# Kernel tuning notes

Hardware: AMD Instinct MI355X
Metric: run time of the kernel (lower is better)

Reference implementation:

```python
import jax, jax.numpy as jnp
import numpy as np

D_MODEL = 1024
NUM_HEADS = 16


def setup_inputs() -> dict:
    key = jax.random.key(0)
    k_x, k_q, k_k, k_v, k_o = jax.random.split(key, 5)
    std = np.sqrt(2.0 / (D_MODEL + D_MODEL))
    x = jax.random.normal(k_x, (2, 2048, D_MODEL), dtype=jnp.float32)
    # LinearLayer stores weight as (out_features, in_features); forward does x @ W.T
    w_q = std * jax.random.truncated_normal(k_q, -2.0, 2.0, (D_MODEL, D_MODEL), dtype=jnp.float32)
    w_k = std * jax.random.truncated_normal(k_k, -2.0, 2.0, (D_MODEL, D_MODEL), dtype=jnp.float32)
    w_v = std * jax.random.truncated_normal(k_v, -2.0, 2.0, (D_MODEL, D_MODEL), dtype=jnp.float32)
    w_o = std * jax.random.truncated_normal(k_o, -2.0, 2.0, (D_MODEL, D_MODEL), dtype=jnp.float32)
    return {"x": x, "w_q": w_q, "w_k": w_k, "w_v": w_v, "w_o": w_o}


def reference(x, w_q, w_k, w_v, w_o):
    B, S, D = x.shape
    H = NUM_HEADS
    dk = D // H
    # projections: x @ W.T
    def split_heads(t):
        return t.reshape(B, S, H, dk).transpose(0, 2, 1, 3)  # (B,H,S,dk)
    q = split_heads(x @ w_q.T)
    k = split_heads(x @ w_k.T)
    v = split_heads(x @ w_v.T)
    scale = 1.0 / np.sqrt(dk).astype(np.float32)
    score = jnp.einsum('bhqd,bhkd->bhqk', q, k) * scale  # (B,H,S,S)
    causal = jnp.tril(jnp.ones((S, S), dtype=bool))
    score = jnp.where(causal[None, None], score, jnp.float32(-jnp.inf))
    attn = jax.nn.softmax(score, axis=-1)
    out = jnp.einsum('bhqk,bhkd->bhqd', attn, v)  # (B,H,S,dk)
    out = out.transpose(0, 2, 1, 3).reshape(B, S, D)
    return out @ w_o.T
```

## Files before the change

### kernel.cpp

```cpp
#include <hip/hip_runtime.h>
#include <hip/hip_bf16.h>
#include <math.h>

typedef float f32x4 __attribute__((ext_vector_type(4)));
typedef short bf16x8_t __attribute__((ext_vector_type(8)));
typedef unsigned short u16;
typedef unsigned int u32;

#define SEQ     2048
#define DMODEL  1024
#define HEADS   16
#define DK      64

__device__ __forceinline__ u16 f2bf(float f) {
    union { float f; unsigned int u; } x; x.f = f;
    unsigned int r = x.u + 0x7fffu + ((x.u >> 16) & 1u);
    return (u16)(r >> 16);
}

__device__ __forceinline__ float bf2f(u16 v) {
    union { u32 u; float f; } x; x.u = ((u32)v) << 16; return x.f;
}

__device__ __forceinline__ int swz(int row) { return ((row ^ (row >> 3)) & 7) << 4; }

__device__ __forceinline__ void gload_lds16(const u16* g, u16* l) {
    __builtin_amdgcn_global_load_lds((const __attribute__((address_space(1))) void*)g,
                                     (__attribute__((address_space(3))) void*)l,
                                     16, 0, 0);
}

__global__ void cvt5(const float* __restrict__ s0, const float* __restrict__ s1,
                     const float* __restrict__ s2, const float* __restrict__ s3,
                     const float* __restrict__ s4,
                     u16* __restrict__ d0, u16* __restrict__ d1, u16* __restrict__ d2,
                     u16* __restrict__ d3, u16* __restrict__ d4,
                     int n0, int n1, int n2, int n3, int n4)
{
    const float* s; u16* d; int n;
    switch (blockIdx.y) {
        case 0: s = s0; d = d0; n = n0; break;
        case 1: s = s1; d = d1; n = n1; break;
        case 2: s = s2; d = d2; n = n2; break;
        case 3: s = s3; d = d3; n = n3; break;
        default: s = s4; d = d4; n = n4; break;
    }
    int i = (blockIdx.x * 256 + threadIdx.x) * 4;
    if (i >= n) return;
    float4 v = *(const float4*)(s + i);
    ushort4 o;
    o.x = f2bf(v.x); o.y = f2bf(v.y); o.z = f2bf(v.z); o.w = f2bf(v.w);
    *(ushort4*)(d + i) = o;
}

template<int OUTBF16, int BN>
__launch_bounds__(256, 2)
__global__ void gemm_bt(const u16* __restrict__ A,
                        const u16* __restrict__ B0, const u16* __restrict__ B1,
                        const u16* __restrict__ B2,
                        void* C0v, void* C1v, void* C2v,
                        int M, int N, int K)
{
    const u16* B = (blockIdx.z == 0) ? B0 : (blockIdx.z == 1 ? B1 : B2);
    void* Cv     = (blockIdx.z == 0) ? C0v : (blockIdx.z == 1 ? C1v : C2v);

    __shared__ u16 Als[128 * 64];
    __shared__ u16 Bls[BN * 64];

    const int tid = threadIdx.x;
    const int w = tid >> 6, l = tid & 63;
    const int rl = l & 15, rh = l >> 4;
    const int row0 = blockIdx.x * 128, col0 = blockIdx.y * BN;
    constexpr int MI = (BN == 128) ? 4 : 2;
    const int wr = (BN == 128) ? (w >> 1) * 64 : w * 32;
    const int wc = (BN == 128) ? (w & 1) * 64 : 0;

    f32x4 acc[MI][4];
    #pragma unroll
    for (int i = 0; i < MI; i++)
        #pragma unroll
        for (int j = 0; j < 4; j++)
            acc[i][j] = (f32x4){0.f, 0.f, 0.f, 0.f};

    for (int kt = 0; kt < K; kt += 64) {
        #pragma unroll
        for (int i = 0; i < 4; i++) {
            int c = i * 256 + tid;
            int r = c >> 3, s = c & 7;
            gload_lds16(A + (size_t)(row0 + r) * K + kt + s * 8, &Als[(i * 256 + w * 64) * 8]);
        }
        #pragma unroll
        for (int i = 0; i < BN / 32; i++) {
            int c = i * 256 + tid;
            int r = c >> 3, s = c & 7;
            gload_lds16(B + (size_t)(col0 + r) * K + kt + s * 8, &Bls[(i * 256 + w * 64) * 8]);
        }
        __syncthreads();

        bf16x8_t af[MI][2], bfr[4][2];
        #pragma unroll
        for (int mi = 0; mi < MI; mi++)
            #pragma unroll
            for (int k0 = 0; k0 < 2; k0++)
                af[mi][k0] = *(const bf16x8_t*)&Als[(wr + mi * 16 + rl) * 64 + k0 * 32 + rh * 8];
        #pragma unroll
        for (int ni = 0; ni < 4; ni++)
            #pragma unroll
            for (int k0 = 0; k0 < 2; k0++)
                bfr[ni][k0] = *(const bf16x8_t*)&Bls[(wc + ni * 16 + rl) * 64 + k0 * 32 + rh * 8];

        #pragma unroll
        for (int mi = 0; mi < MI; mi++)
            #pragma unroll
            for (int ni = 0; ni < 4; ni++)
                #pragma unroll
                for (int k0 = 0; k0 < 2; k0++)
                    acc[mi][ni] = __builtin_amdgcn_mfma_f32_16x16x32_bf16(
                        af[mi][k0], bfr[ni][k0], acc[mi][ni], 0, 0, 0);
        __syncthreads();
    }

    #pragma unroll
    for (int mi = 0; mi < MI; mi++)
        #pragma unroll
        for (int ni = 0; ni < 4; ni++) {
            int r = row0 + wr + mi * 16 + rh * 4;
            int c = col0 + wc + ni * 16 + rl;
            #pragma unroll
            for (int j = 0; j < 4; j++) {
                if (OUTBF16) ((u16*)Cv)[(size_t)(r + j) * N + c] = f2bf(acc[mi][ni][j]);
                else         ((float*)Cv)[(size_t)(r + j) * N + c] = acc[mi][ni][j];
            }
        }
}

__launch_bounds__(256, 4)
__global__ void attn_fwd(const u16* __restrict__ Q, const u16* __restrict__ Kp,
                         const u16* __restrict__ Vp, u16* __restrict__ O)
{
    const int pi = blockIdx.x;
    const int bh = blockIdx.y;
    const int b = bh >> 4, h = bh & 15;
    const int tid = threadIdx.x, w = tid >> 6, l = tid & 63;
    const int rl = l & 15, rh = l >> 4;

    __shared__ u16 Kls[2][64 * 64];
    __shared__ u16 Vt[2][64 * 64];
    __shared__ u16 Pls[4][16 * 64];

    const size_t base = (size_t)b * SEQ * DMODEL + h * DK;
    const float SC = 0.125f * 1.44269504f;
    const int krl8 = l >> 3, ks = l & 7;
    const int rpair = tid >> 3, dseg = tid & 7;

    for (int half = 0; half < 2; half++) {
        const int qti = half ? (31 - pi) : pi;
        const int nt = qti + 1;
        const int qt0 = qti * 64;

        bf16x8_t qf[2];
        #pragma unroll
        for (int k0 = 0; k0 < 2; k0++) {
            int row = qt0 + w * 16 + rl;
            bf16x8_t qr = *(const bf16x8_t*)(Q + base + (size_t)row * DMODEL + k0 * 32 + rh * 8);
            #pragma unroll
            for (int j = 0; j < 8; j++)
                qf[k0][j] = (short)f2bf(bf2f((u16)qr[j]) * SC);
        }

        f32x4 oacc[4];
        float mrun[4], lrun[4];
        #pragma unroll
        for (int nd = 0; nd < 4; nd++) oacc[nd] = (f32x4){0.f, 0.f, 0.f, 0.f};
        #pragma unroll
        for (int j = 0; j < 4; j++) { mrun[j] = -INFINITY; lrun[j] = 0.f; }

        #pragma unroll
        for (int c = 0; c < 2; c++) {
            int kr = w * 16 + c * 8 + krl8;
            int sseg = ks ^ ((kr ^ (kr >> 3)) & 7);
            gload_lds16(Kp + base + (size_t)kr * DMODEL + sseg * 8,
                        &Kls[0][(w * 16 + c * 8) * 64]);
        }
        {
            const u16* vg = Vp + base + (size_t)(2 * rpair) * DMODEL + dseg * 8;
            bf16x8_t v0 = *(const bf16x8_t*)vg;
            bf16x8_t v1 = *(const bf16x8_t*)(vg + DMODEL);
            #pragma unroll
            for (int j = 0; j < 8; j++) {
                int d = dseg * 8 + j;
                u32 pk = (u32)(u16)v0[j] | ((u32)(u16)v1[j] << 16);
                *(u32*)((char*)&Vt[0][0] + ((d * 128 + rpair * 4) ^ swz(d))) = pk;
            }
        }
        __syncthreads();

        for (int t = 0; t < nt; t++) {
            const int cur = t & 1;
            const bool more = (t + 1 < nt);
            bf16x8_t vv0, vv1;

            if (more) {
                #pragma unroll
                for (int c = 0; c < 2; c++) {
                    int kr = w * 16 + c * 8 + krl8;
                    int sseg = ks ^ ((kr ^ (kr >> 3)) & 7);
                    gload_lds16(Kp + base + (size_t)((t + 1) * 64 + kr) * DMODEL + sseg * 8,
                                &Kls[cur ^ 1][(w * 16 + c * 8) * 64]);
                }
                const u16* vg = Vp + base + (size_t)((t + 1) * 64 + 2 * rpair) * DMODEL + dseg * 8;
                vv0 = *(const bf16x8_t*)vg;
                vv1 = *(const bf16x8_t*)(vg + DMODEL);
            }

            f32x4 sa[4];
            #pragma unroll
            for (int ni = 0; ni < 4; ni++) sa[ni] = (f32x4){0.f, 0.f, 0.f, 0.f};
            #pragma unroll
            for (int k0 = 0; k0 < 2; k0++) {
                bf16x8_t kf[4];
                #pragma unroll
                for (int ni = 0; ni < 4; ni++) {
                    int row = ni * 16 + rl;
                    kf[ni] = *(const bf16x8_t*)((const char*)&Kls[cur][0] +
                              (((row * 64 + k0 * 32 + rh * 8) * 2) ^ swz(row)));
                }
                #pragma unroll
                for (int ni = 0; ni < 4; ni++)
                    sa[ni] = __builtin_amdgcn_mfma_f32_16x16x32_bf16(
                        qf[k0], kf[ni], sa[ni], 0, 0, 0);
            }

            const bool diag = (t + 1 == nt);
            float rmax[4], rsum[4];
            #pragma unroll
            for (int j = 0; j < 4; j++) {
                float mx = -INFINITY;
                #pragma unroll
                for (int ni = 0; ni < 4; ni++) {
                    float s = sa[ni][j];
                    if (diag) {
                        s = ((ni * 16 + rl) > (w * 16 + rh * 4 + j)) ? -INFINITY : s;
                        sa[ni][j] = s;
                    }
                    mx = fmaxf(mx, s);
                }
                rmax[j] = mx;
            }
            #pragma unroll
            for (int msk = 1; msk < 16; msk <<= 1)
                #pragma unroll
                for (int j = 0; j < 4; j++)
                    rmax[j] = fmaxf(rmax[j], __shfl_xor(rmax[j], msk, 64));
            #pragma unroll
            for (int j = 0; j < 4; j++) {
                const float mn = fmaxf(mrun[j], rmax[j]);
                const float alpha = exp2f(mrun[j] - mn);
                mrun[j] = mn;
                float rs = 0.f;
                #pragma unroll
                for (int ni = 0; ni < 4; ni++) {
                    float p = exp2f(sa[ni][j] - mn);
                    sa[ni][j] = p;
                    rs += p;
                }
                rsum[j] = rs;
                lrun[j] *= alpha;
                #pragma unroll
                for (int nd = 0; nd < 4; nd++) oacc[nd][j] *= alpha;
            }
            #pragma unroll
            for (int msk = 1; msk < 16; msk <<= 1)
                #pragma unroll
                for (int j = 0; j < 4; j++)
                    rsum[j] += __shfl_xor(rsum[j], msk, 64);
            #pragma unroll
            for (int j = 0; j < 4; j++) lrun[j] += rsum[j];

            #pragma unroll
            for (int ni = 0; ni < 4; ni++)
                #pragma unroll
                for (int j = 0; j < 4; j++) {
                    int row = rh * 4 + j;
                    *(u16*)((char*)&Pls[w][0] +
                            (((row * 64 + ni * 16 + rl) * 2) ^ swz(row))) = f2bf(sa[ni][j]);
                }

            #pragma unroll
            for (int k0 = 0; k0 < 2; k0++) {
                bf16x8_t pf = *(const bf16x8_t*)((const char*)&Pls[w][0] +
                               (((rl * 64 + k0 * 32 + rh * 8) * 2) ^ swz(rl)));
                bf16x8_t vf[4];
                #pragma unroll
                for (int nd = 0; nd < 4; nd++) {
                    int row = nd * 16 + rl;
                    vf[nd] = *(const bf16x8_t*)((const char*)&Vt[cur][0] +
                              (((row * 64 + k0 * 32 + rh * 8) * 2) ^ swz(row)));
                }
                #pragma unroll
                for (int nd = 0; nd < 4; nd++)
                    oacc[nd] = __builtin_amdgcn_mfma_f32_16x16x32_bf16(
                        pf, vf[nd], oacc[nd], 0, 0, 0);
            }

            if (more) {
                #pragma unroll
                for (int j = 0; j < 8; j++) {
                    int d = dseg * 8 + j;
                    u32 pk = (u32)(u16)vv0[j] | ((u32)(u16)vv1[j] << 16);
                    *(u32*)((char*)&Vt[cur ^ 1][0] + ((d * 128 + rpair * 4) ^ swz(d))) = pk;
                }
            }
            __syncthreads();
        }

        #pragma unroll
        for (int nd = 0; nd < 4; nd++)
            #pragma unroll
            for (int j = 0; j < 4; j++) {
                int row = qt0 + w * 16 + rh * 4 + j;
                O[base + (size_t)row * DMODEL + nd * 16 + rl] =
                    f2bf(oacc[nd][j] / lrun[j]);
            }
    }
}

extern "C" void kernel_launch(void* const* d_in, const int* in_sizes, int n_in,
                              void* d_out, int out_size, void* d_ws, size_t ws_size,
                              hipStream_t stream)
{
    const float* x  = (const float*)d_in[0];
    const float* wq = (const float*)d_in[1];
    const float* wk = (const float*)d_in[2];
    const float* wv = (const float*)d_in[3];
    const float* wo = (const float*)d_in[4];
    float* out = (float*)d_out;

    const size_t NX = (size_t)4096 * 1024;
    const size_t NW = (size_t)1024 * 1024;

    u16* xb  = (u16*)d_ws;
    u16* wqb = xb  + NX;
    u16* wkb = wqb + NW;
    u16* wvb = wkb + NW;
    u16* wob = wvb + NW;
    u16* q   = wob + NW;
    u16* k   = q   + NX;
    u16* v   = k   + NX;
    u16* at  = v   + NX;

    cvt5<<<dim3(4096, 5), 256, 0, stream>>>(x, wq, wk, wv, wo,
                                            xb, wqb, wkb, wvb, wob,
                                            (int)NX, (int)NW, (int)NW, (int)NW, (int)NW);

    gemm_bt<1, 128><<<dim3(32, 8, 3), 256, 0, stream>>>(xb, wqb, wkb, wvb,
                                                        q, k, v, 4096, 1024, 1024);

    attn_fwd<<<dim3(16, 32), 256, 0, stream>>>(q, k, v, at);

    gemm_bt<0, 64><<<dim3(32, 16, 1), 256, 0, stream>>>(at, wob, wob, wob,
                                                        out, out, out, 4096, 1024, 1024);
}
```

Before: 230.5 us.

## Transpose QK^T MFMA, lazy softmax rescaling, and remap block indices

The QK^T MFMA now computes S^T by swapping its operands, so each lane holds one query row. Row max and sum then need only two cross-lane shuffles instead of four per value, and P is written to LDS as packed 32-bit pairs. The running max is rescaled only when some row's max grows by more than 8 (log2 domain), which skips most exp and multiply rescales but lets exponents grow up to 2^8 before correction. Block indices are also remapped so that groups of concurrently scheduled blocks share batch-head K/V data.

```diff
diff --git a/kernel.cpp b/kernel.cpp
--- a/kernel.cpp
+++ b/kernel.cpp
@@ -138,8 +138,9 @@
 __global__ void attn_fwd(const u16* __restrict__ Q, const u16* __restrict__ Kp,
                          const u16* __restrict__ Vp, u16* __restrict__ O)
 {
-    const int pi = blockIdx.x;
-    const int bh = blockIdx.y;
+    const int L  = blockIdx.x + (blockIdx.y << 4);
+    const int pi = L >> 5;
+    const int bh = (((L >> 3) & 3) << 3) | (L & 7);
     const int b = bh >> 4, h = bh & 15;
     const int tid = threadIdx.x, w = tid >> 6, l = tid & 63;
     const int rl = l & 15, rh = l >> 4;
@@ -169,11 +170,9 @@
         }
 
         f32x4 oacc[4];
-        float mrun[4], lrun[4];
+        float mrun = -INFINITY, lrun = 0.f;
         #pragma unroll
         for (int nd = 0; nd < 4; nd++) oacc[nd] = (f32x4){0.f, 0.f, 0.f, 0.f};
-        #pragma unroll
-        for (int j = 0; j < 4; j++) { mrun[j] = -INFINITY; lrun[j] = 0.f; }
 
         #pragma unroll
         for (int c = 0; c < 2; c++) {
@@ -228,63 +227,63 @@
                 #pragma unroll
                 for (int ni = 0; ni < 4; ni++)
                     sa[ni] = __builtin_amdgcn_mfma_f32_16x16x32_bf16(
-                        qf[k0], kf[ni], sa[ni], 0, 0, 0);
-            }
-
-            const bool diag = (t + 1 == nt);
-            float rmax[4], rsum[4];
-            #pragma unroll
-            for (int j = 0; j < 4; j++) {
-                float mx = -INFINITY;
-                #pragma unroll
-                for (int ni = 0; ni < 4; ni++) {
-                    float s = sa[ni][j];
-                    if (diag) {
-                        s = ((ni * 16 + rl) > (w * 16 + rh * 4 + j)) ? -INFINITY : s;
-                        sa[ni][j] = s;
-                    }
-                    mx = fmaxf(mx, s);
-                }
-                rmax[j] = mx;
-            }
-            #pragma unroll
-            for (int msk = 1; msk < 16; msk <<= 1)
-                #pragma unroll
-                for (int j = 0; j < 4; j++)
-                    rmax[j] = fmaxf(rmax[j], __shfl_xor(rmax[j], msk, 64));
-            #pragma unroll
-            for (int j = 0; j < 4; j++) {
-                const float mn = fmaxf(mrun[j], rmax[j]);
-                const float alpha = exp2f(mrun[j] - mn);
-                mrun[j] = mn;
-                float rs = 0.f;
-                #pragma unroll
-                for (int ni = 0; ni < 4; ni++) {
-                    float p = exp2f(sa[ni][j] - mn);
+                        kf[ni], qf[k0], sa[ni], 0, 0, 0);
+            }
+
+            if (t + 1 == nt) {
+                const int ql = w * 16 + rl;
+                #pragma unroll
+                for (int ni = 0; ni < 4; ni++)
+                    #pragma unroll
+                    for (int j = 0; j < 4; j++)
+                        if (ni * 16 + rh * 4 + j > ql) sa[ni][j] = -INFINITY;
+            }
+
+            float m0, m1, m2, m3, mx;
+            m0 = fmaxf(fmaxf(sa[0][0], sa[0][1]), fmaxf(sa[0][2], sa[0][3]));
+            m1 = fmaxf(fmaxf(sa[1][0], sa[1][1]), fmaxf(sa[1][2], sa[1][3]));
+            m2 = fmaxf(fmaxf(sa[2][0], sa[2][1]), fmaxf(sa[2][2], sa[2][3]));
+            m3 = fmaxf(fmaxf(sa[3][0], sa[3][1]), fmaxf(sa[3][2], sa[3][3]));
+            mx = fmaxf(fmaxf(m0, m1), fmaxf(m2, m3));
+            mx = fmaxf(mx, __shfl_xor(mx, 16, 64));
+            mx = fmaxf(mx, __shfl_xor(mx, 32, 64));
+
+            if (__any(mx - mrun > 8.f)) {
+                const float mn = fmaxf(mrun, mx);
+                const float alpha = exp2f(mrun - mn);
+                mrun = mn;
+                lrun *= alpha;
+                #pragma unroll
+                for (int j = 0; j < 4; j++) {
+                    float aj = __shfl(alpha, (l & 48) | (rh * 4 + j), 64);
+                    #pragma unroll
+                    for (int nd = 0; nd < 4; nd++) oacc[nd][j] *= aj;
+                }
+            }
+
+            float s0 = 0.f, s1 = 0.f;
+            #pragma unroll
+            for (int ni = 0; ni < 4; ni++) {
+                #pragma unroll
+                for (int j = 0; j < 4; j++) {
+                    float p = exp2f(sa[ni][j] - mrun);
                     sa[ni][j] = p;
-                    rs += p;
-                }
-                rsum[j] = rs;
-                lrun[j] *= alpha;
-                #pragma unroll
-                for (int nd = 0; nd < 4; nd++) oacc[nd][j] *= alpha;
-            }
-            #pragma unroll
-            for (int msk = 1; msk < 16; msk <<= 1)
-                #pragma unroll
-                for (int j = 0; j < 4; j++)
-                    rsum[j] += __shfl_xor(rsum[j], msk, 64);
-            #pragma unroll
-            for (int j = 0; j < 4; j++) lrun[j] += rsum[j];
-
-            #pragma unroll
-            for (int ni = 0; ni < 4; ni++)
-                #pragma unroll
-                for (int j = 0; j < 4; j++) {
-                    int row = rh * 4 + j;
-                    *(u16*)((char*)&Pls[w][0] +
-                            (((row * 64 + ni * 16 + rl) * 2) ^ swz(row))) = f2bf(sa[ni][j]);
-                }
+                    if (ni < 2) s0 += p; else s1 += p;
+                }
+            }
+            float ss = s0 + s1;
+            ss += __shfl_xor(ss, 16, 64);
+            ss += __shfl_xor(ss, 32, 64);
+            lrun += ss;
+
+            #pragma unroll
+            for (int ni = 0; ni < 4; ni++) {
+                u32 p01 = (u32)f2bf(sa[ni][0]) | ((u32)f2bf(sa[ni][1]) << 16);
+                u32 p23 = (u32)f2bf(sa[ni][2]) | ((u32)f2bf(sa[ni][3]) << 16);
+                int col = ni * 16 + rh * 4;
+                *(u32*)((char*)&Pls[w][0] + (((rl * 64 + col) * 2) ^ swz(rl)))     = p01;
+                *(u32*)((char*)&Pls[w][0] + (((rl * 64 + col + 2) * 2) ^ swz(rl))) = p23;
+            }
 
             #pragma unroll
             for (int k0 = 0; k0 < 2; k0++) {
@@ -314,13 +313,17 @@
             __syncthreads();
         }
 
+        float lq[4];
+        #pragma unroll
+        for (int j = 0; j < 4; j++)
+            lq[j] = __shfl(lrun, (l & 48) | (rh * 4 + j), 64);
         #pragma unroll
         for (int nd = 0; nd < 4; nd++)
             #pragma unroll
             for (int j = 0; j < 4; j++) {
                 int row = qt0 + w * 16 + rh * 4 + j;
                 O[base + (size_t)row * DMODEL + nd * 16 + rl] =
-                    f2bf(oacc[nd][j] / lrun[j]);
+                    f2bf(oacc[nd][j] / lq[j]);
             }
     }
 }
```

Result: faster. 197.4 us (-14.4%).
